# Kernel tuning notes

Hardware: AMD Instinct MI355X
Metric: run time of the kernel (lower is better)

The kernel has to match this reference:

```python
import jax, jax.numpy as jnp
import numpy as np
import math

B, S, DM, H = 4, 4096, 1024, 16
HD = DM // H  # 64

def setup_inputs() -> dict:
    key = jax.random.key(0)
    ks = jax.random.split(key, 5)
    def xavier(k, shape):
        bound = math.sqrt(6.0 / (shape[0] + shape[1]))
        return jax.random.uniform(k, shape, jnp.float32, -bound, bound)
    return {
        "x": jax.random.normal(ks[0], (B, S, DM), jnp.float32),
        "Wq": xavier(ks[1], (DM, DM)),
        "Wk": xavier(ks[2], (DM, DM)),
        "Wv": xavier(ks[3], (DM, DM)),
        "Wfc": xavier(ks[4], (DM, DM)),
    }

def reference(x, Wq, Wk, Wv, Wfc):
    b, s, dm = x.shape
    h, hd = H, dm // H
    # nn.Linear(no bias): x @ W.T, then view [B, S, H, HD]
    Q = (x @ Wq.T).reshape(b, s, h, hd)
    K = (x @ Wk.T).reshape(b, s, h, hd)
    V = (x @ Wv.T).reshape(b, s, h, hd)
    # NOTE: faithful to original — no head transpose, so attention is over heads axis.
    # scores: [B, S, H, H]
    scores = jnp.einsum('bshd,bstd->bsht', Q, K) / math.sqrt(hd)
    attn = jax.nn.softmax(scores, axis=-1)
    # dropout is identity in eval mode
    out = jnp.einsum('bsht,bstd->bshd', attn, V).reshape(b, s, dm)
    return out @ Wfc.T
```

## Files before the change

### kernel.cpp

```cpp
#include <hip/hip_runtime.h>

typedef unsigned short u16;
typedef unsigned int u32;
typedef short bf16x8 __attribute__((ext_vector_type(8)));
typedef float f32x4 __attribute__((ext_vector_type(4)));

__device__ __forceinline__ u16 f2bf(float f) {
    u32 u = __float_as_uint(f);
    u32 r = (u + 0x7fffu + ((u >> 16) & 1u)) >> 16;
    return (u16)r;
}

__device__ __forceinline__ void gld_lds16(const void* g, void* s) {
    __builtin_amdgcn_global_load_lds(
        (__attribute__((address_space(1))) void*)(g),
        (__attribute__((address_space(3))) void*)(s),
        16, 0, 0);
}

__global__ void cast_all(const float* __restrict__ x,
                         const float* __restrict__ wq, const float* __restrict__ wk,
                         const float* __restrict__ wv, const float* __restrict__ wfc,
                         u16* __restrict__ xb, u16* __restrict__ wqkvb, u16* __restrict__ wfcb) {
    size_t g = (size_t)blockIdx.x * 256 + threadIdx.x;
    const float* s;
    u16* d;
    size_t off;
    if (g < 4194304u) {
        s = x; d = xb; off = g;
    } else {
        size_t w = g - 4194304u;
        int y = (int)(w >> 18);
        off = w & 262143u;
        s = (y == 0) ? wq : (y == 1) ? wk : (y == 2) ? wv : wfc;
        d = (y < 3) ? (wqkvb + (size_t)y * 1048576u) : wfcb;
    }
    float4 v = ((const float4*)s)[off];
    ushort4 o;
    o.x = f2bf(v.x); o.y = f2bf(v.y); o.z = f2bf(v.z); o.w = f2bf(v.w);
    *(ushort4*)(d + off * 4) = o;
}

template <int MODE>
__global__ __launch_bounds__(512, 2)
void gemm_bt8(const u16* __restrict__ A, const u16* __restrict__ B,
              void* __restrict__ C0, void* __restrict__ C1,
              int M, int N, int K) {
    __shared__ __align__(16) u16 sA[4][8192];
    __shared__ __align__(16) u16 sB[4][8192];

    const int tid  = threadIdx.x;
    const int lane = tid & 63;
    const int wave = tid >> 6;
    const int wm = wave >> 2;
    const int wn = wave & 3;

    const int ntx = N >> 8;
    const int cpx = gridDim.x >> 3;
    const int swz = ((int)blockIdx.x & 7) * cpx + ((int)blockIdx.x >> 3);
    const int bm = (swz / ntx) << 8;
    const int bn = (swz % ntx) << 8;

    const int srow = tid >> 2;
    const int sch  = (tid & 3) ^ ((srow >> 1) & 3);
    const u16* a0 = A + (size_t)(bm +       srow) * K + sch * 8;
    const u16* a1 = A + (size_t)(bm + 128 + srow) * K + sch * 8;
    const u16* b0 = B + (size_t)(bn +       srow) * K + sch * 8;
    const u16* b1 = B + (size_t)(bn + 128 + srow) * K + sch * 8;
    const int ldst = tid * 8;

    auto stA = [&](int t) {
        u16* d = &sA[t & 3][0];
        gld_lds16(a0 + t * 32, d + ldst);
        gld_lds16(a1 + t * 32, d + 4096 + ldst);
    };
    auto stB = [&](int t) {
        u16* d = &sB[t & 3][0];
        gld_lds16(b0 + t * 32, d + ldst);
        gld_lds16(b1 + t * 32, d + 4096 + ldst);
    };

    const int l15 = lane & 15;
    const int sc8 = (((lane >> 4) ^ ((l15 >> 1) & 3)) << 3);
    const int arow = wm * 128 + l15;
    const int brow = wn * 64  + l15;

    f32x4 acc[8][4];
#pragma unroll
    for (int i = 0; i < 8; ++i)
#pragma unroll
        for (int j = 0; j < 4; ++j) acc[i][j] = (f32x4){0.f, 0.f, 0.f, 0.f};

    const int T = K >> 5;

    stA(0); stB(0); stA(1); stB(1); stA(2); stB(2);
    asm volatile("s_waitcnt vmcnt(8)" ::: "memory");
    asm volatile("s_barrier" ::: "memory");

    for (int w = 0; w < T; ++w) {
        const u16* pa = &sA[w & 3][0];
        const u16* pb = &sB[w & 3][0];

        bf16x8 af[4], bf[4];
#pragma unroll
        for (int i = 0; i < 4; ++i)
            af[i] = *(const bf16x8*)&pa[(arow + i * 16) * 32 + sc8];
#pragma unroll
        for (int j = 0; j < 4; ++j)
            bf[j] = *(const bf16x8*)&pb[(brow + j * 16) * 32 + sc8];
        if (w + 3 < T) stA(w + 3);
        asm volatile("s_barrier" ::: "memory");
        asm volatile("s_waitcnt lgkmcnt(0)" ::: "memory");
        __builtin_amdgcn_s_setprio(1);
#pragma unroll
        for (int i = 0; i < 4; ++i)
#pragma unroll
            for (int j = 0; j < 4; ++j)
                acc[i][j] = __builtin_amdgcn_mfma_f32_16x16x32_bf16(
                    af[i], bf[j], acc[i][j], 0, 0, 0);
        __builtin_amdgcn_s_setprio(0);
        asm volatile("s_barrier" ::: "memory");

        bf16x8 ag[4];
#pragma unroll
        for (int i = 0; i < 4; ++i)
            ag[i] = *(const bf16x8*)&pa[(arow + (i + 4) * 16) * 32 + sc8];
        if (w + 3 < T) stB(w + 3);
        if (w < T - 3)       asm volatile("s_waitcnt vmcnt(8)" ::: "memory");
        else if (w == T - 3) asm volatile("s_waitcnt vmcnt(4)" ::: "memory");
        else if (w == T - 2) asm volatile("s_waitcnt vmcnt(0)" ::: "memory");
        asm volatile("s_barrier" ::: "memory");
        asm volatile("s_waitcnt lgkmcnt(0)" ::: "memory");
        __builtin_amdgcn_s_setprio(1);
#pragma unroll
        for (int i = 0; i < 4; ++i)
#pragma unroll
            for (int j = 0; j < 4; ++j)
                acc[i + 4][j] = __builtin_amdgcn_mfma_f32_16x16x32_bf16(
                    ag[i], bf[j], acc[i + 4][j], 0, 0, 0);
        __builtin_amdgcn_s_setprio(0);
        asm volatile("s_barrier" ::: "memory");
    }

    const int cr = (lane >> 4) * 4;
    const int cc = l15;
#pragma unroll
    for (int i = 0; i < 8; ++i) {
#pragma unroll
        for (int j = 0; j < 4; ++j) {
            const int row0 = bm + wm * 128 + i * 16 + cr;
            const int col  = bn + wn * 64 + j * 16 + cc;
#pragma unroll
            for (int r = 0; r < 4; ++r) {
                float v = acc[i][j][r];
                const int row = row0 + r;
                if (MODE == 0) {
                    if (col < 2048)
                        ((u16*)C0)[(size_t)row * 2048 + col] = f2bf(v);
                    else
                        ((u16*)C1)[(size_t)row * 1024 + (col - 2048)] = f2bf(v);
                } else {
                    ((float*)C0)[(size_t)row * N + col] = v;
                }
            }
        }
    }
}

__global__ __launch_bounds__(256)
void attn_kernel(const u16* __restrict__ QK, const u16* __restrict__ V,
                 u16* __restrict__ O) {
    __shared__ __align__(16) u16 sQ[4][16 * 80];
    __shared__ __align__(16) u16 sK[4][16 * 80];
    __shared__ __align__(16) u16 sV[4][64 * 16];
    __shared__ __align__(16) u16 sP[4][16 * 16];

    const int lane = threadIdx.x & 63;
    const int wave = threadIdx.x >> 6;
    const size_t m = (size_t)blockIdx.x * 4 + wave;
    const u16* bqk = QK + m * 2048;
    const u16* bv  = V + m * 1024;

#pragma unroll
    for (int c6 = 0; c6 < 4; ++c6) {
        int chunk = c6 * 64 + lane;
        uint4 v = *(const uint4*)(bqk + chunk * 8);
        int cc = chunk & 127;
        int row = cc >> 3, pch = cc & 7;
        u16* dst = (chunk < 128) ? sQ[wave] : sK[wave];
        *(uint4*)&dst[row * 80 + pch * 8] = v;
    }
#pragma unroll
    for (int c6 = 0; c6 < 2; ++c6) {
        int cc = c6 * 64 + lane;
        int t = cc >> 3, d0 = (cc & 7) * 8;
        uint4 v = *(const uint4*)(bv + cc * 8);
        u16 e[8]; *(uint4*)e = v;
#pragma unroll
        for (int k = 0; k < 8; ++k) {
            int d = d0 + k;
            int blk = (t >> 3) ^ ((d >> 3) & 1);
            sV[wave][d * 16 + blk * 8 + (t & 7)] = e[k];
        }
    }
    __syncthreads();

    const int ln = lane & 15;
    const int g  = lane >> 4;

    f32x4 s = (f32x4){0.f, 0.f, 0.f, 0.f};
    {
        bf16x8 a0 = *(const bf16x8*)&sK[wave][ln * 80 + g * 8];
        bf16x8 b0 = *(const bf16x8*)&sQ[wave][ln * 80 + g * 8];
        s = __builtin_amdgcn_mfma_f32_16x16x32_bf16(a0, b0, s, 0, 0, 0);
        bf16x8 a1 = *(const bf16x8*)&sK[wave][ln * 80 + 32 + g * 8];
        bf16x8 b1 = *(const bf16x8*)&sQ[wave][ln * 80 + 32 + g * 8];
        s = __builtin_amdgcn_mfma_f32_16x16x32_bf16(a1, b1, s, 0, 0, 0);
    }
    float sv[4];
#pragma unroll
    for (int r = 0; r < 4; ++r) sv[r] = s[r] * 0.125f;

    float mx = fmaxf(fmaxf(sv[0], sv[1]), fmaxf(sv[2], sv[3]));
    mx = fmaxf(mx, __shfl_xor(mx, 16));
    mx = fmaxf(mx, __shfl_xor(mx, 32));
    float e[4], sum = 0.f;
#pragma unroll
    for (int r = 0; r < 4; ++r) { e[r] = __expf(sv[r] - mx); sum += e[r]; }
    sum += __shfl_xor(sum, 16);
    sum += __shfl_xor(sum, 32);
    const float inv = 1.f / sum;

    ushort4 pb;
    pb.x = f2bf(e[0] * inv); pb.y = f2bf(e[1] * inv);
    pb.z = f2bf(e[2] * inv); pb.w = f2bf(e[3] * inv);
    *(ushort4*)&sP[wave][ln * 16 + g * 4] = pb;
    __syncthreads();

    bf16x8 bl = *(const bf16x8*)&sP[wave][ln * 16 + (g & 1) * 8];
    bf16x8 bz = (bf16x8){0, 0, 0, 0, 0, 0, 0, 0};
    bf16x8 bp = (g < 2) ? bl : bz;

#pragma unroll
    for (int dt = 0; dt < 4; ++dt) {
        int d = dt * 16 + ln;
        int blk = (g & 1) ^ ((d >> 3) & 1);
        bf16x8 av = *(const bf16x8*)&sV[wave][d * 16 + blk * 8];
        f32x4 o = __builtin_amdgcn_mfma_f32_16x16x32_bf16(
            av, bp, (f32x4){0.f, 0.f, 0.f, 0.f}, 0, 0, 0);
        ushort4 ob;
        ob.x = f2bf(o[0]); ob.y = f2bf(o[1]);
        ob.z = f2bf(o[2]); ob.w = f2bf(o[3]);
        *(ushort4*)(O + m * 1024 + ln * 64 + dt * 16 + g * 4) = ob;
    }
}

extern "C" void kernel_launch(void* const* d_in, const int* in_sizes, int n_in,
                              void* d_out, int out_size, void* d_ws, size_t ws_size,
                              hipStream_t stream) {
    const float* x   = (const float*)d_in[0];
    const float* Wq  = (const float*)d_in[1];
    const float* Wk  = (const float*)d_in[2];
    const float* Wv  = (const float*)d_in[3];
    const float* Wfc = (const float*)d_in[4];

    const int M = 16384, K = 1024, NQKV = 3072, N2 = 1024;

    char* ws = (char*)d_ws;
    u16* xb    = (u16*)ws;
    u16* wqkvb = (u16*)(ws + 33554432);
    u16* wfcb  = (u16*)(ws + 33554432 + 6291456);
    u16* vbuf  = (u16*)(ws + 33554432 + 6291456 + 2097152);
    u16* qkbuf = (u16*)d_out;

    cast_all<<<20480, 256, 0, stream>>>(x, Wq, Wk, Wv, Wfc, xb, wqkvb, wfcb);

    gemm_bt8<0><<<768, 512, 0, stream>>>(xb, wqkvb, qkbuf, vbuf, M, NQKV, K);

    u16* Ob = xb;
    attn_kernel<<<M / 4, 256, 0, stream>>>(qkbuf, vbuf, Ob);

    gemm_bt8<1><<<256, 512, 0, stream>>>(Ob, wfcb, d_out, nullptr, M, N2, K);
}
```

Before: 296.5 us.

## Use simpler 128x128 GEMM for QKV projection and stage attention output via LDS

Adds a simpler single-buffered 128x128-tile GEMM with BK=64 and switches the QKV projection to it in place of the 256x256 four-stage pipelined kernel. In the attention kernel, Q and K are now read straight from global memory into MFMA operands instead of being staged through LDS. The attention output is also staged through LDS so it can be written to global memory as coalesced 16-byte stores. The new GEMM drops the multi-stage prefetch and gets less reuse per tile, which risks lower MFMA throughput on the largest GEMM.

```diff
diff --git a/kernel.cpp b/kernel.cpp
--- a/kernel.cpp
+++ b/kernel.cpp
@@ -4,6 +4,8 @@
 typedef unsigned int u32;
 typedef short bf16x8 __attribute__((ext_vector_type(8)));
 typedef float f32x4 __attribute__((ext_vector_type(4)));
+
+#define BN 128
 
 __device__ __forceinline__ u16 f2bf(float f) {
     u32 u = __float_as_uint(f);
@@ -41,114 +43,75 @@
     *(ushort4*)(d + off * 4) = o;
 }
 
-template <int MODE>
-__global__ __launch_bounds__(512, 2)
-void gemm_bt8(const u16* __restrict__ A, const u16* __restrict__ B,
-              void* __restrict__ C0, void* __restrict__ C1,
-              int M, int N, int K) {
-    __shared__ __align__(16) u16 sA[4][8192];
-    __shared__ __align__(16) u16 sB[4][8192];
+template <int BMT, int MODE>
+__global__ __launch_bounds__(256, 2)
+void gemm_bt(const u16* __restrict__ A, const u16* __restrict__ B,
+             void* __restrict__ C0, void* __restrict__ C1, int M, int N, int K) {
+    constexpr int WMT = BMT / 32;
+    __shared__ __align__(16) u16 As[BMT * 64];
+    __shared__ __align__(16) u16 Bs[BN * 64];
 
     const int tid  = threadIdx.x;
     const int lane = tid & 63;
     const int wave = tid >> 6;
-    const int wm = wave >> 2;
-    const int wn = wave & 3;
-
-    const int ntx = N >> 8;
-    const int cpx = gridDim.x >> 3;
-    const int swz = ((int)blockIdx.x & 7) * cpx + ((int)blockIdx.x >> 3);
-    const int bm = (swz / ntx) << 8;
-    const int bn = (swz % ntx) << 8;
-
-    const int srow = tid >> 2;
-    const int sch  = (tid & 3) ^ ((srow >> 1) & 3);
-    const u16* a0 = A + (size_t)(bm +       srow) * K + sch * 8;
-    const u16* a1 = A + (size_t)(bm + 128 + srow) * K + sch * 8;
-    const u16* b0 = B + (size_t)(bn +       srow) * K + sch * 8;
-    const u16* b1 = B + (size_t)(bn + 128 + srow) * K + sch * 8;
-    const int ldst = tid * 8;
-
-    auto stA = [&](int t) {
-        u16* d = &sA[t & 3][0];
-        gld_lds16(a0 + t * 32, d + ldst);
-        gld_lds16(a1 + t * 32, d + 4096 + ldst);
-    };
-    auto stB = [&](int t) {
-        u16* d = &sB[t & 3][0];
-        gld_lds16(b0 + t * 32, d + ldst);
-        gld_lds16(b1 + t * 32, d + 4096 + ldst);
-    };
-
-    const int l15 = lane & 15;
-    const int sc8 = (((lane >> 4) ^ ((l15 >> 1) & 3)) << 3);
-    const int arow = wm * 128 + l15;
-    const int brow = wn * 64  + l15;
-
-    f32x4 acc[8][4];
-#pragma unroll
-    for (int i = 0; i < 8; ++i)
+    const int wm = wave >> 1, wn = wave & 1;
+    const int bm = blockIdx.y * BMT;
+    const int bn = blockIdx.x * BN;
+
+    const int srow   = lane >> 3;
+    const int schunk = (lane & 7) ^ srow;
+
+    f32x4 acc[WMT][4];
+#pragma unroll
+    for (int i = 0; i < WMT; ++i)
 #pragma unroll
         for (int j = 0; j < 4; ++j) acc[i][j] = (f32x4){0.f, 0.f, 0.f, 0.f};
 
-    const int T = K >> 5;
-
-    stA(0); stB(0); stA(1); stB(1); stA(2); stB(2);
-    asm volatile("s_waitcnt vmcnt(8)" ::: "memory");
-    asm volatile("s_barrier" ::: "memory");
-
-    for (int w = 0; w < T; ++w) {
-        const u16* pa = &sA[w & 3][0];
-        const u16* pb = &sB[w & 3][0];
-
-        bf16x8 af[4], bf[4];
-#pragma unroll
-        for (int i = 0; i < 4; ++i)
-            af[i] = *(const bf16x8*)&pa[(arow + i * 16) * 32 + sc8];
-#pragma unroll
-        for (int j = 0; j < 4; ++j)
-            bf[j] = *(const bf16x8*)&pb[(brow + j * 16) * 32 + sc8];
-        if (w + 3 < T) stA(w + 3);
-        asm volatile("s_barrier" ::: "memory");
-        asm volatile("s_waitcnt lgkmcnt(0)" ::: "memory");
-        __builtin_amdgcn_s_setprio(1);
-#pragma unroll
-        for (int i = 0; i < 4; ++i)
-#pragma unroll
-            for (int j = 0; j < 4; ++j)
-                acc[i][j] = __builtin_amdgcn_mfma_f32_16x16x32_bf16(
-                    af[i], bf[j], acc[i][j], 0, 0, 0);
-        __builtin_amdgcn_s_setprio(0);
-        asm volatile("s_barrier" ::: "memory");
-
-        bf16x8 ag[4];
-#pragma unroll
-        for (int i = 0; i < 4; ++i)
-            ag[i] = *(const bf16x8*)&pa[(arow + (i + 4) * 16) * 32 + sc8];
-        if (w + 3 < T) stB(w + 3);
-        if (w < T - 3)       asm volatile("s_waitcnt vmcnt(8)" ::: "memory");
-        else if (w == T - 3) asm volatile("s_waitcnt vmcnt(4)" ::: "memory");
-        else if (w == T - 2) asm volatile("s_waitcnt vmcnt(0)" ::: "memory");
-        asm volatile("s_barrier" ::: "memory");
-        asm volatile("s_waitcnt lgkmcnt(0)" ::: "memory");
-        __builtin_amdgcn_s_setprio(1);
-#pragma unroll
-        for (int i = 0; i < 4; ++i)
-#pragma unroll
-            for (int j = 0; j < 4; ++j)
-                acc[i + 4][j] = __builtin_amdgcn_mfma_f32_16x16x32_bf16(
-                    ag[i], bf[j], acc[i + 4][j], 0, 0, 0);
-        __builtin_amdgcn_s_setprio(0);
-        asm volatile("s_barrier" ::: "memory");
+    const int nkt = K >> 6;
+    for (int kt = 0; kt < nkt; ++kt) {
+        const int k0 = kt << 6;
+        __syncthreads();
+#pragma unroll
+        for (int j = 0; j < WMT; ++j) {
+            const int r = j * 32 + wave * 8;
+            gld_lds16(A + (size_t)(bm + r + srow) * K + k0 + schunk * 8, &As[r * 64]);
+        }
+#pragma unroll
+        for (int j = 0; j < 4; ++j) {
+            const int r = j * 32 + wave * 8;
+            gld_lds16(B + (size_t)(bn + r + srow) * K + k0 + schunk * 8, &Bs[r * 64]);
+        }
+        __syncthreads();
+#pragma unroll
+        for (int kk = 0; kk < 2; ++kk) {
+            const int c = kk * 4 + (lane >> 4);
+            bf16x8 af[WMT], bfr[4];
+#pragma unroll
+            for (int i = 0; i < WMT; ++i) {
+                int m = wm * (WMT * 16) + i * 16 + (lane & 15);
+                af[i] = *(const bf16x8*)&As[m * 64 + ((c ^ (m & 7)) << 3)];
+            }
+#pragma unroll
+            for (int j = 0; j < 4; ++j) {
+                int n = wn * 64 + j * 16 + (lane & 15);
+                bfr[j] = *(const bf16x8*)&Bs[n * 64 + ((c ^ (n & 7)) << 3)];
+            }
+#pragma unroll
+            for (int i = 0; i < WMT; ++i)
+#pragma unroll
+                for (int j = 0; j < 4; ++j)
+                    acc[i][j] = __builtin_amdgcn_mfma_f32_16x16x32_bf16(
+                        af[i], bfr[j], acc[i][j], 0, 0, 0);
+        }
     }
 
     const int cr = (lane >> 4) * 4;
-    const int cc = l15;
-#pragma unroll
-    for (int i = 0; i < 8; ++i) {
+    const int cc = lane & 15;
+#pragma unroll
+    for (int i = 0; i < WMT; ++i) {
 #pragma unroll
         for (int j = 0; j < 4; ++j) {
-            const int row0 = bm + wm * 128 + i * 16 + cr;
+            const int row0 = bm + wm * (WMT * 16) + i * 16 + cr;
             const int col  = bn + wn * 64 + j * 16 + cc;
 #pragma unroll
             for (int r = 0; r < 4; ++r) {
@@ -167,13 +130,138 @@
     }
 }
 
+template <int MODE>
+__global__ __launch_bounds__(512, 2)
+void gemm_bt8(const u16* __restrict__ A, const u16* __restrict__ B,
+              void* __restrict__ C0, void* __restrict__ C1,
+              int M, int N, int K) {
+    __shared__ __align__(16) u16 sA[4][8192];
+    __shared__ __align__(16) u16 sB[4][8192];
+
+    const int tid  = threadIdx.x;
+    const int lane = tid & 63;
+    const int wave = tid >> 6;
+    const int wm = wave >> 2;
+    const int wn = wave & 3;
+
+    const int ntx = N >> 8;
+    const int cpx = gridDim.x >> 3;
+    const int swz = ((int)blockIdx.x & 7) * cpx + ((int)blockIdx.x >> 3);
+    const int bm = (swz / ntx) << 8;
+    const int bn = (swz % ntx) << 8;
+
+    const int srow = tid >> 2;
+    const int sch  = (tid & 3) ^ ((srow >> 1) & 3);
+    const u16* a0 = A + (size_t)(bm +       srow) * K + sch * 8;
+    const u16* a1 = A + (size_t)(bm + 128 + srow) * K + sch * 8;
+    const u16* b0 = B + (size_t)(bn +       srow) * K + sch * 8;
+    const u16* b1 = B + (size_t)(bn + 128 + srow) * K + sch * 8;
+    const int ldst = tid * 8;
+
+    auto stA = [&](int t) {
+        u16* d = &sA[t & 3][0];
+        gld_lds16(a0 + t * 32, d + ldst);
+        gld_lds16(a1 + t * 32, d + 4096 + ldst);
+    };
+    auto stB = [&](int t) {
+        u16* d = &sB[t & 3][0];
+        gld_lds16(b0 + t * 32, d + ldst);
+        gld_lds16(b1 + t * 32, d + 4096 + ldst);
+    };
+
+    const int l15 = lane & 15;
+    const int sc8 = (((lane >> 4) ^ ((l15 >> 1) & 3)) << 3);
+    const int arow = wm * 128 + l15;
+    const int brow = wn * 64  + l15;
+
+    f32x4 acc[8][4];
+#pragma unroll
+    for (int i = 0; i < 8; ++i)
+#pragma unroll
+        for (int j = 0; j < 4; ++j) acc[i][j] = (f32x4){0.f, 0.f, 0.f, 0.f};
+
+    const int T = K >> 5;
+
+    stA(0); stB(0); stA(1); stB(1); stA(2); stB(2);
+    asm volatile("s_waitcnt vmcnt(8)" ::: "memory");
+    asm volatile("s_barrier" ::: "memory");
+
+    for (int w = 0; w < T; ++w) {
+        const u16* pa = &sA[w & 3][0];
+        const u16* pb = &sB[w & 3][0];
+
+        bf16x8 af[4], bf[4];
+#pragma unroll
+        for (int i = 0; i < 4; ++i)
+            af[i] = *(const bf16x8*)&pa[(arow + i * 16) * 32 + sc8];
+#pragma unroll
+        for (int j = 0; j < 4; ++j)
+            bf[j] = *(const bf16x8*)&pb[(brow + j * 16) * 32 + sc8];
+        if (w + 3 < T) stA(w + 3);
+        asm volatile("s_barrier" ::: "memory");
+        asm volatile("s_waitcnt lgkmcnt(0)" ::: "memory");
+        __builtin_amdgcn_s_setprio(1);
+#pragma unroll
+        for (int i = 0; i < 4; ++i)
+#pragma unroll
+            for (int j = 0; j < 4; ++j)
+                acc[i][j] = __builtin_amdgcn_mfma_f32_16x16x32_bf16(
+                    af[i], bf[j], acc[i][j], 0, 0, 0);
+        __builtin_amdgcn_s_setprio(0);
+        asm volatile("s_barrier" ::: "memory");
+
+        bf16x8 ag[4];
+#pragma unroll
+        for (int i = 0; i < 4; ++i)
+            ag[i] = *(const bf16x8*)&pa[(arow + (i + 4) * 16) * 32 + sc8];
+        if (w + 3 < T) stB(w + 3);
+        if (w < T - 3)       asm volatile("s_waitcnt vmcnt(8)" ::: "memory");
+        else if (w == T - 3) asm volatile("s_waitcnt vmcnt(4)" ::: "memory");
+        else if (w == T - 2) asm volatile("s_waitcnt vmcnt(0)" ::: "memory");
+        asm volatile("s_barrier" ::: "memory");
+        asm volatile("s_waitcnt lgkmcnt(0)" ::: "memory");
+        __builtin_amdgcn_s_setprio(1);
+#pragma unroll
+        for (int i = 0; i < 4; ++i)
+#pragma unroll
+            for (int j = 0; j < 4; ++j)
+                acc[i + 4][j] = __builtin_amdgcn_mfma_f32_16x16x32_bf16(
+                    ag[i], bf[j], acc[i + 4][j], 0, 0, 0);
+        __builtin_amdgcn_s_setprio(0);
+        asm volatile("s_barrier" ::: "memory");
+    }
+
+    const int cr = (lane >> 4) * 4;
+    const int cc = l15;
+#pragma unroll
+    for (int i = 0; i < 8; ++i) {
+#pragma unroll
+        for (int j = 0; j < 4; ++j) {
+            const int row0 = bm + wm * 128 + i * 16 + cr;
+            const int col  = bn + wn * 64 + j * 16 + cc;
+#pragma unroll
+            for (int r = 0; r < 4; ++r) {
+                float v = acc[i][j][r];
+                const int row = row0 + r;
+                if (MODE == 0) {
+                    if (col < 2048)
+                        ((u16*)C0)[(size_t)row * 2048 + col] = f2bf(v);
+                    else
+                        ((u16*)C1)[(size_t)row * 1024 + (col - 2048)] = f2bf(v);
+                } else {
+                    ((float*)C0)[(size_t)row * N + col] = v;
+                }
+            }
+        }
+    }
+}
+
 __global__ __launch_bounds__(256)
 void attn_kernel(const u16* __restrict__ QK, const u16* __restrict__ V,
                  u16* __restrict__ O) {
-    __shared__ __align__(16) u16 sQ[4][16 * 80];
-    __shared__ __align__(16) u16 sK[4][16 * 80];
     __shared__ __align__(16) u16 sV[4][64 * 16];
-    __shared__ __align__(16) u16 sP[4][16 * 16];
+    __shared__ __align__(16) u16 sP[4][256];
+    __shared__ __align__(16) u16 sO[4][1152];
 
     const int lane = threadIdx.x & 63;
     const int wave = threadIdx.x >> 6;
@@ -182,15 +270,6 @@
     const u16* bv  = V + m * 1024;
 
 #pragma unroll
-    for (int c6 = 0; c6 < 4; ++c6) {
-        int chunk = c6 * 64 + lane;
-        uint4 v = *(const uint4*)(bqk + chunk * 8);
-        int cc = chunk & 127;
-        int row = cc >> 3, pch = cc & 7;
-        u16* dst = (chunk < 128) ? sQ[wave] : sK[wave];
-        *(uint4*)&dst[row * 80 + pch * 8] = v;
-    }
-#pragma unroll
     for (int c6 = 0; c6 < 2; ++c6) {
         int cc = c6 * 64 + lane;
         int t = cc >> 3, d0 = (cc & 7) * 8;
@@ -203,19 +282,16 @@
             sV[wave][d * 16 + blk * 8 + (t & 7)] = e[k];
         }
     }
-    __syncthreads();
 
     const int ln = lane & 15;
     const int g  = lane >> 4;
 
     f32x4 s = (f32x4){0.f, 0.f, 0.f, 0.f};
     {
-        bf16x8 a0 = *(const bf16x8*)&sK[wave][ln * 80 + g * 8];
-        bf16x8 b0 = *(const bf16x8*)&sQ[wave][ln * 80 + g * 8];
-        s = __builtin_amdgcn_mfma_f32_16x16x32_bf16(a0, b0, s, 0, 0, 0);
-        bf16x8 a1 = *(const bf16x8*)&sK[wave][ln * 80 + 32 + g * 8];
-        bf16x8 b1 = *(const bf16x8*)&sQ[wave][ln * 80 + 32 + g * 8];
-        s = __builtin_amdgcn_mfma_f32_16x16x32_bf16(a1, b1, s, 0, 0, 0);
+        const bf16x8* kb = (const bf16x8*)(bqk + 1024 + ln * 64 + g * 8);
+        const bf16x8* qb = (const bf16x8*)(bqk +        ln * 64 + g * 8);
+        s = __builtin_amdgcn_mfma_f32_16x16x32_bf16(kb[0], qb[0], s, 0, 0, 0);
+        s = __builtin_amdgcn_mfma_f32_16x16x32_bf16(kb[4], qb[4], s, 0, 0, 0);
     }
     float sv[4];
 #pragma unroll
@@ -251,7 +327,15 @@
         ushort4 ob;
         ob.x = f2bf(o[0]); ob.y = f2bf(o[1]);
         ob.z = f2bf(o[2]); ob.w = f2bf(o[3]);
-        *(ushort4*)(O + m * 1024 + ln * 64 + dt * 16 + g * 4) = ob;
+        *(ushort4*)&sO[wave][ln * 72 + dt * 16 + g * 4] = ob;
+    }
+    __syncthreads();
+
+#pragma unroll
+    for (int c6 = 0; c6 < 2; ++c6) {
+        int c = c6 * 64 + lane;
+        uint4 v = *(const uint4*)&sO[wave][(c >> 3) * 72 + (c & 7) * 8];
+        *(uint4*)(O + m * 1024 + c * 8) = v;
     }
 }
 
@@ -275,7 +359,8 @@
 
     cast_all<<<20480, 256, 0, stream>>>(x, Wq, Wk, Wv, Wfc, xb, wqkvb, wfcb);
 
-    gemm_bt8<0><<<768, 512, 0, stream>>>(xb, wqkvb, qkbuf, vbuf, M, NQKV, K);
+    gemm_bt<128, 0><<<dim3(NQKV / BN, M / 128), 256, 0, stream>>>(
+        xb, wqkvb, qkbuf, vbuf, M, NQKV, K);
 
     u16* Ob = xb;
     attn_kernel<<<M / 4, 256, 0, stream>>>(qkbuf, vbuf, Ob);
```

Result: faster. 286.5 us (-3.4%).
